# Performance work log

Measured on AMD Instinct MI355X. Metric: run time of the kernel, lower is better.

Reference implementation:

```python
import jax, jax.numpy as jnp
import numpy as np

B, T, C, H = 4, 2048, 1024, 64  # batch, seq, embedding_size, head_size

def setup_inputs() -> dict:
    key = jax.random.key(0)
    k0, k1, k2, k3 = jax.random.split(key, 4)
    scale = 0.02
    return {
        "x":  jax.random.normal(k0, (B, T, C), dtype=jnp.float32),
        "Wq": jax.random.normal(k1, (H, C), dtype=jnp.float32) * scale,
        "Wk": jax.random.normal(k2, (H, C), dtype=jnp.float32) * scale,
        "Wv": jax.random.normal(k3, (H, C), dtype=jnp.float32) * scale,
    }

def reference(x, Wq, Wk, Wv):
    # Linear(bias=False): y = x @ W^T
    q = jnp.einsum('btc,hc->bth', x, Wq)
    k = jnp.einsum('btc,hc->bth', x, Wk)
    v = jnp.einsum('btc,hc->bth', x, Wv)
    # NOTE: original scales by embedding_size C**-0.5, not head_size
    wei = jnp.einsum('bth,bsh->bts', q, k) * (x.shape[-1] ** -0.5)
    t = x.shape[1]
    causal_mask = jnp.tril(jnp.ones((t, t), dtype=bool))  # [T, T]
    wei = jnp.where(causal_mask, wei, -jnp.inf)
    wei = jax.nn.softmax(wei, axis=-1)
    # dropout = 0.0 -> identity (eval mode)
    out = jnp.einsum('bts,bsh->bth', wei, v)
    return out
```

## Files before the change

### kernel.cpp

```cpp
#include <hip/hip_runtime.h>
#include <hip/hip_bf16.h>

typedef unsigned short u16;
typedef __attribute__((ext_vector_type(8))) __bf16 bf16x8;
typedef __attribute__((ext_vector_type(4))) float f32x4;

#define B_ 4
#define T_ 2048
#define C_ 1024
#define H_ 64
#define NSEG 8

__device__ __forceinline__ u16 f2bf(float f) {
    union { __hip_bfloat16 h; u16 u; } cv;
    cv.h = __float2bfloat16(f);
    return cv.u;
}

__device__ __forceinline__ float bf2f(unsigned v) {
    union { unsigned u; float f; } c; c.u = v << 16; return c.f;
}

__device__ __forceinline__ bf16x8 cvt8r(float4 f0, float4 f1) {
    union { u16 h[8]; bf16x8 v; } ua;
    ua.h[0] = f2bf(f0.x); ua.h[1] = f2bf(f0.y);
    ua.h[2] = f2bf(f0.z); ua.h[3] = f2bf(f0.w);
    ua.h[4] = f2bf(f1.x); ua.h[5] = f2bf(f1.y);
    ua.h[6] = f2bf(f1.z); ua.h[7] = f2bf(f1.w);
    return ua.v;
}

__device__ __forceinline__ void gll16(const void* g, void* l) {
    __builtin_amdgcn_global_load_lds(
        (const __attribute__((address_space(1))) void*)g,
        (__attribute__((address_space(3))) void*)l, 16, 0, 0);
}

__global__ __launch_bounds__(256) void wcvt(
    const float* __restrict__ wq, const float* __restrict__ wk,
    const float* __restrict__ wv, u16* __restrict__ wcat)
{
    int e = (blockIdx.x * 256 + threadIdx.x) * 4;
    int row = e >> 10, col = e & 1023;
    const float* src = (row < 64) ? (wq + (size_t)row * C_)
                     : (row < 128) ? (wk + (size_t)(row - 64) * C_)
                                   : (wv + (size_t)(row - 128) * C_);
    float4 f = *(const float4*)(src + col);
    u16 o[4] = { f2bf(f.x), f2bf(f.y), f2bf(f.z), f2bf(f.w) };
    *(uint2*)(wcat + e) = *(uint2*)o;
}

__global__ __launch_bounds__(512) void qkv(
    const float* __restrict__ x, const u16* __restrict__ wcat,
    u16* __restrict__ qP, u16* __restrict__ kP, u16* __restrict__ vP)
{
    __shared__ __align__(16) char smem[65536];

    const int tid = threadIdx.x;
    const int ln  = tid & 63;
    const int w   = tid >> 6;
    const int m0  = blockIdx.x * 32;

    const int lr = ln & 15;
    const int g  = ln >> 4;
    const int ms = w >> 2;
    const int nh = w & 3;

    f32x4 acc[3] = {};

    char (*lds)[32768] = (char(*)[32768])smem;
    const int xrow = w * 4 + (ln >> 4);
    const int xc   = (ln & 15) ^ (xrow & 7);
    const int wseg0 = w * 3;
    const int wlr   = ln >> 3;
    const int wc    = (ln & 7) ^ wlr;

#define STAGE(BUF, KC)                                                         \
    do {                                                                       \
        gll16(x + (size_t)(m0 + xrow) * C_ + (KC) * 64 + xc * 4,               \
              &lds[BUF][w * 1024]);                                            \
        _Pragma("unroll")                                                      \
        for (int i_ = 0; i_ < 3; ++i_) {                                       \
            int s_ = wseg0 + i_;                                               \
            gll16(wcat + (size_t)(s_ * 8 + wlr) * C_ + (KC) * 64 + wc * 8,     \
                  &lds[BUF][8192 + s_ * 1024]);                                \
        }                                                                      \
    } while (0)

    STAGE(0, 0);
    __syncthreads();

    const int ra  = ms * 16 + lr;
    const int rsw = ra & 7;

    for (int kc = 0; kc < 16; ++kc) {
        const int buf = kc & 1;
        if (kc < 15) STAGE(buf ^ 1, kc + 1);

        const char* rb = &lds[buf][0];
        const char* wb = &lds[buf][8192];

        bf16x8 a[2];
        #pragma unroll
        for (int ks = 0; ks < 2; ++ks) {
            int c0 = ks * 8 + g * 2;
            float4 fa = *(const float4*)(rb + ra * 256 + ((c0       ^ rsw) << 4));
            float4 fb = *(const float4*)(rb + ra * 256 + (((c0 + 1) ^ rsw) << 4));
            a[ks] = cvt8r(fa, fb);
        }

        #pragma unroll
        for (int j = 0; j < 3; ++j) {
            int rr = nh * 48 + j * 16 + lr;
            #pragma unroll
            for (int ks = 0; ks < 2; ++ks) {
                int c = (ks * 4 + g) ^ (lr & 7);
                bf16x8 b = *(const bf16x8*)(wb + rr * 128 + c * 16);
                acc[j] = __builtin_amdgcn_mfma_f32_16x16x32_bf16(a[ks], b, acc[j], 0, 0, 0);
            }
        }

        __syncthreads();
    }
#undef STAGE

    float* tile = (float*)smem;
    #pragma unroll
    for (int j = 0; j < 3; ++j)
        #pragma unroll
        for (int i = 0; i < 4; ++i)
            tile[(ms * 16 + g * 4 + i) * 201 + nh * 48 + j * 16 + lr] = acc[j][i];
    __syncthreads();

    for (int uu = tid; uu < 768; uu += 512) {
        const int ln2 = uu & 63;
        const int lr2 = ln2 & 15;
        const int g2  = ln2 >> 4;
        if (uu < 512) {
            const int isK = uu >> 8;
            const int rem = uu & 255;
            const int u   = rem >> 7;
            const int ks  = (rem >> 6) & 1;
            const float* src = tile + (u * 16 + lr2) * 201 + isK * 64 + ks * 32 + g2 * 8;
            float4 f0 = *(const float4*)src;
            float4 f1 = *(const float4*)(src + 4);
            bf16x8 val = cvt8r(f0, f1);
            u16* dst = (isK ? kP : qP)
                     + ((size_t)(((m0 >> 4) + u) * 2 + ks) * 64 + ln2) * 8;
            *(bf16x8*)dst = val;
        } else {
            const int rem = uu - 512;
            const int jf  = rem >> 6;
            union { u16 h[8]; bf16x8 v; } ua;
            #pragma unroll
            for (int e = 0; e < 8; ++e)
                ua.h[e] = f2bf(tile[(g2 * 8 + e) * 201 + 128 + jf * 16 + lr2]);
            u16* dst = vP + ((size_t)((m0 >> 5) * 4 + jf) * 64 + ln2) * 8;
            *(bf16x8*)dst = ua.v;
        }
    }
}

__global__ __launch_bounds__(64) void attn_part(
    const u16* __restrict__ qP, const u16* __restrict__ kP,
    const u16* __restrict__ vP, u16* __restrict__ opart,
    float* __restrict__ ml)
{
    __shared__ u16 ps[16 * 72];

    const int lane = threadIdx.x;
    const int bid  = blockIdx.x;
    const int seg  = bid & (NSEG - 1);
    const int tix  = bid >> 3;
    const int b    = tix & 3;
    const int qt   = 127 - (tix >> 2);
    const int q0   = qt * 16;

    const int lr = lane & 15;
    const int g  = lane >> 4;
    const int lk = g * 8;

    const int nch = (qt >> 2) + 1;
    const int L   = (nch + NSEG - 1) >> 3;
    const int c0  = seg * L;
    const int c1  = min(nch, c0 + L);

    if (c0 >= c1) {
        if (lr == 0)
            #pragma unroll
            for (int i = 0; i < 4; ++i) {
                ml[(size_t)bid * 32 + (g * 4 + i) * 2]     = -1e30f;
                ml[(size_t)bid * 32 + (g * 4 + i) * 2 + 1] = 0.f;
            }
        return;
    }

    bf16x8 aq[2];
    #pragma unroll
    for (int ks = 0; ks < 2; ++ks)
        aq[ks] = *(const bf16x8*)(qP + ((size_t)((b * 128 + qt) * 2 + ks) * 64 + lane) * 8);

    f32x4 oacc[4] = {};
    float mrow[4], lrow[4];
    #pragma unroll
    for (int i = 0; i < 4; ++i) { mrow[i] = -1e30f; lrow[i] = 0.f; }

    for (int jc = c0; jc < c1; ++jc) {
        const int kv0 = jc << 6;

        bf16x8 bk[8];
        #pragma unroll
        for (int jf = 0; jf < 4; ++jf)
            #pragma unroll
            for (int ks = 0; ks < 2; ++ks)
                bk[jf * 2 + ks] = *(const bf16x8*)(kP +
                    ((size_t)((b * 128 + (kv0 >> 4) + jf) * 2 + ks) * 64 + lane) * 8);

        f32x4 sacc[4] = {};
        #pragma unroll
        for (int jf = 0; jf < 4; ++jf)
            #pragma unroll
            for (int ks = 0; ks < 2; ++ks)
                sacc[jf] = __builtin_amdgcn_mfma_f32_16x16x32_bf16(aq[ks], bk[jf * 2 + ks], sacc[jf], 0, 0, 0);

        bf16x8 bv[8];
        #pragma unroll
        for (int ks2 = 0; ks2 < 2; ++ks2)
            #pragma unroll
            for (int jf = 0; jf < 4; ++jf)
                bv[jf * 2 + ks2] = *(const bf16x8*)(vP +
                    ((size_t)((b * 64 + (kv0 >> 5) + ks2) * 4 + jf) * 64 + lane) * 8);

        const bool full = (kv0 + 63 <= q0);
        #pragma unroll
        for (int jf = 0; jf < 4; ++jf) {
            int col = kv0 + jf * 16 + lr;
            #pragma unroll
            for (int i = 0; i < 4; ++i) {
                int row = q0 + g * 4 + i;
                float val = sacc[jf][i] * 0.03125f;
                sacc[jf][i] = (full || col <= row) ? val : -1e30f;
            }
        }

        float pnew[4][4];
        #pragma unroll
        for (int i = 0; i < 4; ++i) {
            float mx = fmaxf(fmaxf(sacc[0][i], sacc[1][i]), fmaxf(sacc[2][i], sacc[3][i]));
            mx = fmaxf(mx, __shfl_xor(mx, 1));
            mx = fmaxf(mx, __shfl_xor(mx, 2));
            mx = fmaxf(mx, __shfl_xor(mx, 4));
            mx = fmaxf(mx, __shfl_xor(mx, 8));
            float mnew = fmaxf(mrow[i], mx);
            float corr = __expf(mrow[i] - mnew);
            float rs = 0.f;
            #pragma unroll
            for (int jf = 0; jf < 4; ++jf) {
                float p = __expf(sacc[jf][i] - mnew);
                pnew[jf][i] = p;
                rs += p;
            }
            rs += __shfl_xor(rs, 1);
            rs += __shfl_xor(rs, 2);
            rs += __shfl_xor(rs, 4);
            rs += __shfl_xor(rs, 8);
            lrow[i] = lrow[i] * corr + rs;
            mrow[i] = mnew;
            #pragma unroll
            for (int jf = 0; jf < 4; ++jf) oacc[jf][i] *= corr;
        }

        #pragma unroll
        for (int jf = 0; jf < 4; ++jf)
            #pragma unroll
            for (int i = 0; i < 4; ++i)
                ps[(g * 4 + i) * 72 + jf * 16 + lr] = f2bf(pnew[jf][i]);

        #pragma unroll
        for (int ks2 = 0; ks2 < 2; ++ks2) {
            bf16x8 ap = *(const bf16x8*)(ps + lr * 72 + ks2 * 32 + lk);
            #pragma unroll
            for (int jf = 0; jf < 4; ++jf)
                oacc[jf] = __builtin_amdgcn_mfma_f32_16x16x32_bf16(ap, bv[jf * 2 + ks2], oacc[jf], 0, 0, 0);
        }
    }

    #pragma unroll
    for (int jf = 0; jf < 4; ++jf)
        #pragma unroll
        for (int i = 0; i < 4; ++i)
            opart[(size_t)bid * 1024 + (g * 4 + i) * 64 + jf * 16 + lr] = f2bf(oacc[jf][i]);
    if (lr == 0)
        #pragma unroll
        for (int i = 0; i < 4; ++i) {
            ml[(size_t)bid * 32 + (g * 4 + i) * 2]     = mrow[i];
            ml[(size_t)bid * 32 + (g * 4 + i) * 2 + 1] = lrow[i];
        }
}

__global__ __launch_bounds__(256) void attn_reduce(
    const u16* __restrict__ opart, const float* __restrict__ ml,
    float* __restrict__ out)
{
    const int t   = blockIdx.x;
    const int row = threadIdx.x >> 4;
    const int p   = threadIdx.x & 15;
    const int b   = t & 3;
    const int qt  = 127 - (t >> 2);

    float m[NSEG], l[NSEG];
    #pragma unroll
    for (int s = 0; s < NSEG; ++s) {
        m[s] = ml[(size_t)(t * NSEG + s) * 32 + row * 2];
        l[s] = ml[(size_t)(t * NSEG + s) * 32 + row * 2 + 1];
    }
    float M = m[0];
    #pragma unroll
    for (int s = 1; s < NSEG; ++s) M = fmaxf(M, m[s]);

    float a0 = 0.f, a1 = 0.f, a2 = 0.f, a3 = 0.f, Lsum = 0.f;
    #pragma unroll
    for (int s = 0; s < NSEG; ++s) {
        float wgt = __expf(m[s] - M);
        Lsum += l[s] * wgt;
        uint2 o = *(const uint2*)(opart + (size_t)(t * NSEG + s) * 1024 + row * 64 + p * 4);
        a0 += wgt * bf2f(o.x & 0xffffu);
        a1 += wgt * bf2f(o.x >> 16);
        a2 += wgt * bf2f(o.y & 0xffffu);
        a3 += wgt * bf2f(o.y >> 16);
    }
    float inv = 1.f / Lsum;
    float4 r; r.x = a0 * inv; r.y = a1 * inv; r.z = a2 * inv; r.w = a3 * inv;
    *(float4*)(out + ((size_t)b * T_ + qt * 16 + row) * H_ + p * 4) = r;
}

extern "C" void kernel_launch(void* const* d_in, const int* in_sizes, int n_in,
                              void* d_out, int out_size, void* d_ws, size_t ws_size,
                              hipStream_t stream) {
    const float* x  = (const float*)d_in[0];
    const float* wq = (const float*)d_in[1];
    const float* wk = (const float*)d_in[2];
    const float* wv = (const float*)d_in[3];

    u16* qPws = (u16*)d_ws;
    u16* kPws = qPws + (size_t)B_ * T_ * H_;
    u16* vPws = kPws + (size_t)B_ * T_ * H_;
    u16* wcat = vPws + (size_t)B_ * T_ * H_;
    u16* opart = wcat + (size_t)192 * C_;
    float* mlbuf = (float*)(opart + (size_t)4096 * 1024);

    wcvt<<<192, 256, 0, stream>>>(wq, wk, wv, wcat);
    qkv<<<256, 512, 0, stream>>>(x, wcat, qPws, kPws, vPws);
    attn_part<<<4096, 64, 0, stream>>>(qPws, kPws, vPws, opart, mlbuf);
    attn_reduce<<<512, 256, 0, stream>>>(opart, mlbuf, (float*)d_out);
}
```

Before: 40.57 us.

## Prepack weights into MFMA fragment layout and read B operands directly from global

```diff
diff --git a/kernel.cpp b/kernel.cpp
--- a/kernel.cpp
+++ b/kernel.cpp
@@ -36,25 +36,30 @@
         (__attribute__((address_space(3))) void*)l, 16, 0, 0);
 }
 
-__global__ __launch_bounds__(256) void wcvt(
+__global__ __launch_bounds__(256) void wpack(
     const float* __restrict__ wq, const float* __restrict__ wk,
-    const float* __restrict__ wv, u16* __restrict__ wcat)
+    const float* __restrict__ wv, u16* __restrict__ wP)
 {
-    int e = (blockIdx.x * 256 + threadIdx.x) * 4;
-    int row = e >> 10, col = e & 1023;
-    const float* src = (row < 64) ? (wq + (size_t)row * C_)
-                     : (row < 128) ? (wk + (size_t)(row - 64) * C_)
-                                   : (wv + (size_t)(row - 128) * C_);
-    float4 f = *(const float4*)(src + col);
-    u16 o[4] = { f2bf(f.x), f2bf(f.y), f2bf(f.z), f2bf(f.w) };
-    *(uint2*)(wcat + e) = *(uint2*)o;
+    int u    = blockIdx.x * 256 + threadIdx.x;
+    int ln   = u & 63;
+    int frag = u >> 6;
+    int ksg  = frag & 31;
+    int j16  = frag >> 5;
+    int n    = j16 * 16 + (ln & 15);
+    int kb   = ksg * 32 + (ln >> 4) * 8;
+    const float* src = (n < 64) ? (wq + (size_t)n * C_)
+                     : (n < 128) ? (wk + (size_t)(n - 64) * C_)
+                                 : (wv + (size_t)(n - 128) * C_);
+    float4 f0 = *(const float4*)(src + kb);
+    float4 f1 = *(const float4*)(src + kb + 4);
+    *(bf16x8*)(wP + (size_t)u * 8) = cvt8r(f0, f1);
 }
 
 __global__ __launch_bounds__(512) void qkv(
-    const float* __restrict__ x, const u16* __restrict__ wcat,
+    const float* __restrict__ x, const u16* __restrict__ wP,
     u16* __restrict__ qP, u16* __restrict__ kP, u16* __restrict__ vP)
 {
-    __shared__ __align__(16) char smem[65536];
+    __shared__ __align__(16) char smem[32768];
 
     const int tid = threadIdx.x;
     const int ln  = tid & 63;
@@ -68,37 +73,25 @@
 
     f32x4 acc[3] = {};
 
-    char (*lds)[32768] = (char(*)[32768])smem;
     const int xrow = w * 4 + (ln >> 4);
     const int xc   = (ln & 15) ^ (xrow & 7);
-    const int wseg0 = w * 3;
-    const int wlr   = ln >> 3;
-    const int wc    = (ln & 7) ^ wlr;
-
-#define STAGE(BUF, KC)                                                         \
-    do {                                                                       \
-        gll16(x + (size_t)(m0 + xrow) * C_ + (KC) * 64 + xc * 4,               \
-              &lds[BUF][w * 1024]);                                            \
-        _Pragma("unroll")                                                      \
-        for (int i_ = 0; i_ < 3; ++i_) {                                       \
-            int s_ = wseg0 + i_;                                               \
-            gll16(wcat + (size_t)(s_ * 8 + wlr) * C_ + (KC) * 64 + wc * 8,     \
-                  &lds[BUF][8192 + s_ * 1024]);                                \
-        }                                                                      \
-    } while (0)
+
+#define STAGE(BUF, KC)                                                     \
+    gll16(x + (size_t)(m0 + xrow) * C_ + (KC) * 64 + xc * 4,               \
+          smem + (BUF) * 8192 + w * 1024)
 
     STAGE(0, 0);
     __syncthreads();
 
     const int ra  = ms * 16 + lr;
     const int rsw = ra & 7;
+    const u16* wbase = wP + (size_t)(nh * 3) * 32 * 64 * 8;
 
     for (int kc = 0; kc < 16; ++kc) {
         const int buf = kc & 1;
         if (kc < 15) STAGE(buf ^ 1, kc + 1);
 
-        const char* rb = &lds[buf][0];
-        const char* wb = &lds[buf][8192];
+        const char* rb = smem + buf * 8192;
 
         bf16x8 a[2];
         #pragma unroll
@@ -111,11 +104,10 @@
 
         #pragma unroll
         for (int j = 0; j < 3; ++j) {
-            int rr = nh * 48 + j * 16 + lr;
             #pragma unroll
             for (int ks = 0; ks < 2; ++ks) {
-                int c = (ks * 4 + g) ^ (lr & 7);
-                bf16x8 b = *(const bf16x8*)(wb + rr * 128 + c * 16);
+                size_t fragofs = ((size_t)(j * 32 + kc * 2 + ks) * 64 + ln) * 8;
+                bf16x8 b = *(const bf16x8*)(wbase + fragofs);
                 acc[j] = __builtin_amdgcn_mfma_f32_16x16x32_bf16(a[ks], b, acc[j], 0, 0, 0);
             }
         }
@@ -345,12 +337,12 @@
     u16* qPws = (u16*)d_ws;
     u16* kPws = qPws + (size_t)B_ * T_ * H_;
     u16* vPws = kPws + (size_t)B_ * T_ * H_;
-    u16* wcat = vPws + (size_t)B_ * T_ * H_;
-    u16* opart = wcat + (size_t)192 * C_;
+    u16* wPws = vPws + (size_t)B_ * T_ * H_;
+    u16* opart = wPws + (size_t)192 * C_;
     float* mlbuf = (float*)(opart + (size_t)4096 * 1024);
 
-    wcvt<<<192, 256, 0, stream>>>(wq, wk, wv, wcat);
-    qkv<<<256, 512, 0, stream>>>(x, wcat, qPws, kPws, vPws);
+    wpack<<<96, 256, 0, stream>>>(wq, wk, wv, wPws);
+    qkv<<<256, 512, 0, stream>>>(x, wPws, qPws, kPws, vPws);
     attn_part<<<4096, 64, 0, stream>>>(qPws, kPws, vPws, opart, mlbuf);
     attn_reduce<<<512, 256, 0, stream>>>(opart, mlbuf, (float*)d_out);
 }
```

Measured after the change: 41.14 us. About the same (+1.4%).
